# Optimization experiments

Measured on AMD Instinct MI355X. Metric: run time of the kernel, lower is better.

## Reference

```python
import math
import jax, jax.numpy as jnp
import numpy as np

B, C, H, W = 8, 256, 32, 32
NH, DK, DV = 8, 32, 32
EPS = 1e-6


def mish(x):
    return x * jnp.tanh(jax.nn.softplus(x))


def grouped_conv1x1(x, w, b, groups):
    # x: (B, Cin, N); w: (Cout, Cin//groups); b: (Cout,)
    Bb, Cin, N = x.shape
    Cout = w.shape[0]
    xg = x.reshape(Bb, groups, Cin // groups, N)
    wg = w.reshape(groups, Cout // groups, Cin // groups)
    y = jnp.einsum('bgin,goi->bgon', xg, wg).reshape(Bb, Cout, N)
    return y + b[None, :, None]


def conv_block(x, w, b, s, beta, groups):
    # 1x1 conv -> BatchNorm (eval: running mean 0 / var 1 => affine) -> Mish
    y = grouped_conv1x1(x, w, b, groups)
    y = s[None, :, None] * y + beta[None, :, None]
    return mish(y)


def setup_inputs() -> dict:
    key = jax.random.key(0)
    ks = jax.random.split(key, 8)
    inp = {
        'x': jax.random.normal(ks[0], (B, C, H, W), dtype=jnp.float32),
        'q_w': jax.random.normal(ks[1], (NH * DK, C // NH), dtype=jnp.float32) * 0.05,
        'q_b': jnp.zeros((NH * DK,), jnp.float32),
        'q_s': jnp.ones((NH * DK,), jnp.float32),
        'q_beta': jnp.zeros((NH * DK,), jnp.float32),
        'k_w': jax.random.normal(ks[2], (NH * DK, C // NH), dtype=jnp.float32) * 0.05,
        'k_b': jnp.zeros((NH * DK,), jnp.float32),
        'k_s': jnp.ones((NH * DK,), jnp.float32),
        'k_beta': jnp.zeros((NH * DK,), jnp.float32),
        'v_w': jax.random.normal(ks[3], (NH * DV, C // NH), dtype=jnp.float32) * 0.05,
        'v_b': jnp.zeros((NH * DV,), jnp.float32),
        'v_s': jnp.ones((NH * DV,), jnp.float32),
        'v_beta': jnp.zeros((NH * DV,), jnp.float32),
        'f_w': jax.random.normal(ks[4], (C, NH * DV), dtype=jnp.float32) * 0.05,
        'f_b': jnp.zeros((C,), jnp.float32),
        'f_s': jnp.ones((C,), jnp.float32),
        'f_beta': jnp.zeros((C,), jnp.float32),
    }
    return inp


def _forward(x, q_w, q_b, q_s, q_beta, k_w, k_b, k_s, k_beta,
             v_w, v_b, v_s, v_beta, f_w, f_b, f_s, f_beta):
    b, c, h, w = x.shape
    n = h * w
    temp = math.sqrt(c / NH)
    xf = x.reshape(b, c, n)

    q = conv_block(xf, q_w, q_b, q_s, q_beta, NH).reshape(b, NH, DK, n) / temp
    k = conv_block(xf, k_w, k_b, k_s, k_beta, NH).reshape(b, NH, DK, n)
    v = conv_block(xf, v_w, v_b, v_s, v_beta, NH).reshape(b, NH, DV, n)

    # cosine-distance attention (all heads vectorized); identical math to the
    # torch broadcast/repeat version but computed via normalized dot products.
    qn = jnp.sqrt(jnp.sum(q * q, axis=2))  # (b, nh, n)
    kn = jnp.sqrt(jnp.sum(k * k, axis=2))
    dot = jnp.einsum('bhdn,bhdm->bhnm', q, k)  # (b, nh, n, n)
    denom = jnp.maximum(qn[:, :, :, None] * kn[:, :, None, :], EPS)
    cos = jnp.clip(dot / denom, -1.0 + 1e-6, 1.0 - 1e-6)
    attn = jax.nn.softmax(1.0 - jnp.arccos(cos) / math.pi, axis=-1)

    # out[..., d, i] = sum_m v[..., d, m] * attn[..., i, m]
    out = jnp.einsum('bhdm,bhnm->bhdn', v, attn).reshape(b, NH * DV, n)

    y = conv_block(out, f_w, f_b, f_s, f_beta, 1).reshape(b, c, h, w) + x

    # extract_attn_map (no_grad in original)
    am = jnp.sum(jnp.mean(attn, axis=1), axis=1)  # (b, n)
    mn = jnp.min(am, axis=1, keepdims=True)
    mx = jnp.max(am, axis=1, keepdims=True)
    am = ((am - mn) / (mx - mn)).reshape(b, h, w)
    return y, jax.lax.stop_gradient(am)


def reference(x, q_w, q_b, q_s, q_beta, k_w, k_b, k_s, k_beta,
              v_w, v_b, v_s, v_beta, f_w, f_b, f_s, f_beta):
    return _forward(x, q_w, q_b, q_s, q_beta, k_w, k_b, k_s, k_beta,
                    v_w, v_b, v_s, v_beta, f_w, f_b, f_s, f_beta)
```

## Files before the change

kernel.cpp:

```cpp
#include <hip/hip_runtime.h>
#include <math.h>

#define B_   8
#define C_   256
#define NH_  8
#define N_   1024
#define LOG2E    1.4426950408889634f

typedef __attribute__((ext_vector_type(8))) short bf16x8;
typedef __attribute__((ext_vector_type(4))) float f32x4;
typedef __attribute__((ext_vector_type(2))) float f32x2;
typedef unsigned short u16;
typedef unsigned int u32;

#define AS1 __attribute__((address_space(1)))
#define AS3 __attribute__((address_space(3)))

__device__ __forceinline__ f32x4 mfma16(bf16x8 a, bf16x8 b, f32x4 c) {
    return __builtin_amdgcn_mfma_f32_16x16x32_bf16(a, b, c, 0, 0, 0);
}
__device__ __forceinline__ u32 bf16r(float x) {
    u32 b = __float_as_uint(x);
    return (b + 0x7fffu + ((b >> 16) & 1u)) >> 16;
}
__device__ __forceinline__ float mish_fast(float x) {
    float e  = __builtin_amdgcn_exp2f(fminf(x, 30.f) * LOG2E);
    float nm = e * (e + 2.f);
    return x * nm * __builtin_amdgcn_rcpf(nm + 2.f);
}
__device__ __forceinline__ f32x2 splat2(float v) { return (f32x2){v, v}; }
__device__ __forceinline__ f32x2 fexp_poly2(f32x2 c) {
    c = __builtin_elementwise_min(
            __builtin_elementwise_max(c, splat2(-0.999999f)), splat2(0.999999f));
    f32x2 u = c * c;
    f32x2 p = __builtin_elementwise_fma(splat2(1.7809920f), u, splat2(-3.7571968f));
    f32x2 q = __builtin_elementwise_fma(splat2(6.3713280f), u, splat2(-15.1427584f));
    p = __builtin_elementwise_fma(p, u, splat2(2.8140000f));
    q = __builtin_elementwise_fma(q, u, splat2(13.1518784f));
    p = __builtin_elementwise_fma(p, u, splat2(-0.8122592f));
    q = __builtin_elementwise_fma(q, u, splat2(-4.8903712f));
    p = __builtin_elementwise_fma(p, u, splat2(0.1705120f));
    q = __builtin_elementwise_fma(q, u, splat2(0.8441120f));
    p = __builtin_elementwise_fma(p, u, splat2(1.6473155f));
    q = __builtin_elementwise_fma(q, u, splat2(0.4936541f));
    return __builtin_elementwise_fma(c, q, p);
}

__global__ __launch_bounds__(256) void qkvpack_kernel(
    const float* __restrict__ x,
    const float* __restrict__ qw, const float* __restrict__ qb2,
    const float* __restrict__ qs, const float* __restrict__ qbeta,
    const float* __restrict__ kw, const float* __restrict__ kb2,
    const float* __restrict__ ks, const float* __restrict__ kbeta,
    const float* __restrict__ vw, const float* __restrict__ vb2,
    const float* __restrict__ vs, const float* __restrict__ vbeta,
    uint4* __restrict__ qpk, uint4* __restrict__ kpk, u16* __restrict__ vbf,
    const float* __restrict__ fw, u16* __restrict__ wbf)
{
    int blk = blockIdx.x;
    if (blk >= 768) {
        int id = (blk - 768) * 1024 + threadIdx.x;
#pragma unroll
        for (int j = 0; j < 4; ++j) { int p = id + j * 256; wbf[p] = (u16)bf16r(fw[p]); }
        return;
    }
    int type = blk >> 8;
    int sub = blk & 255;
    int nt = sub & 3, g = (sub >> 2) & 7, b = sub >> 5;
    int n = nt * 256 + threadIdx.x;
    int bh = b * 8 + g;
    const float* xp = x + ((size_t)b * C_ + g * 32) * N_ + n;
    float xv[32];
#pragma unroll
    for (int i = 0; i < 32; ++i) xv[i] = xp[(size_t)i * N_];

    const float *w, *bb, *sc, *bt;
    if (type == 0)      { w = qw; bb = qb2; sc = qs; bt = qbeta; }
    else if (type == 1) { w = kw; bb = kb2; sc = ks; bt = kbeta; }
    else                { w = vw; bb = vb2; sc = vs; bt = vbeta; }

    float y[32];
#pragma unroll
    for (int co = 0; co < 32; ++co) {
        int cg = g * 32 + co;
        float acc = 0.f;
#pragma unroll
        for (int i = 0; i < 32; ++i)
            acc = fmaf(xv[i], w[cg * 32 + i], acc);
        y[co] = mish_fast(sc[cg] * (acc + bb[cg]) + bt[cg]);
    }

    if (type == 2) {
#pragma unroll
        for (int co = 0; co < 32; ++co)
            vbf[((size_t)bh * 32 + co) * N_ + n] = (u16)bf16r(y[co]);
        return;
    }
    float s2 = 0.f;
#pragma unroll
    for (int d = 0; d < 32; ++d) s2 = fmaf(y[d], y[d], s2);
    float inv = __builtin_amdgcn_rsqf(fmaxf(s2, 1e-24f));
    u32 wp[16];
#pragma unroll
    for (int d = 0; d < 16; ++d)
        wp[d] = bf16r(y[2 * d] * inv) | (bf16r(y[2 * d + 1] * inv) << 16);
    uint4* dst = (type == 0 ? qpk : kpk) + ((size_t)bh * N_ + n) * 4;
#pragma unroll
    for (int j = 0; j < 4; ++j)
        dst[j] = make_uint4(wp[4 * j], wp[4 * j + 1], wp[4 * j + 2], wp[4 * j + 3]);
}

__global__ __launch_bounds__(256) void attn_kernel(
    const u16* __restrict__ qpk, const u16* __restrict__ kpk,
    const u16* __restrict__ vbf,
    u16* __restrict__ aout_bt, float* __restrict__ ampart)
{
    __shared__ __align__(16) u16 Kc[512 * 8];
    __shared__ __align__(16) u16 Vc[512 * 8];
    __shared__ __align__(16) u16 Ps[4][16 * 136];

    const int tid  = threadIdx.x;
    const int wave = tid >> 6, lane = tid & 63;
    const int l15 = lane & 15, lg = lane >> 4;
    const int swz = (blockIdx.x & 7) * 128 + (blockIdx.x >> 3);
    const int itile = swz & 15, bh = swz >> 4;
    const int h = bh & 7, bidx = bh >> 3;
    const int i0 = itile * 64;

    const char* ksrc = (const char*)(kpk + (size_t)bh * N_ * 32);
    const char* vsrc = (const char*)(vbf + (size_t)bh * 32 * N_);
    const char* qsrc = (const char*)(qpk + (size_t)bh * N_ * 32);

    const int kj0 = tid >> 7, km0g = tid & 127;
    const int kj1 = (256 + tid) >> 7, km1g = (256 + tid) & 127;
    const int vd0 = tid >> 4, vg0 = tid & 15;
    const int vd1 = (256 + tid) >> 4, vg1 = (256 + tid) & 15;
    const size_t koff0 = (size_t)km0g * 64 + kj0 * 16;
    const size_t koff1 = (size_t)km1g * 64 + kj1 * 16;
    const size_t voff0 = (size_t)vd0 * 2048 + ((vg0 ^ (vd0 & 7)) << 4);
    const size_t voff1 = (size_t)vd1 * 2048 + ((vg1 ^ (vd1 & 7)) << 4);

    bf16x8 aq = *(const bf16x8*)(qsrc + (size_t)(i0 + wave * 16 + l15) * 64 + lg * 16);

    const char* kfb = (const char*)Kc + lg * 2048 + l15 * 16;

    uint4 kreg0 = *(const uint4*)(ksrc + koff0);
    uint4 kreg1 = *(const uint4*)(ksrc + koff1);
    f32x2 rsL = {0.f, 0.f}, rsH = {0.f, 0.f};
    for (int ch = 0; ch < 8; ++ch) {
        *(uint4*)((char*)Kc + tid * 16)         = kreg0;
        *(uint4*)((char*)Kc + (256 + tid) * 16) = kreg1;
        if (ch < 7) {
            kreg0 = *(const uint4*)(ksrc + (size_t)(ch + 1) * 8192 + koff0);
            kreg1 = *(const uint4*)(ksrc + (size_t)(ch + 1) * 8192 + koff1);
        }
        asm volatile("s_waitcnt lgkmcnt(0)" ::: "memory");
        __builtin_amdgcn_sched_barrier(0);
        __builtin_amdgcn_s_barrier();
        __builtin_amdgcn_sched_barrier(0);
#pragma unroll
        for (int t = 0; t < 8; ++t) {
            bf16x8 bk = *(const bf16x8*)(kfb + t * 256);
            f32x4 cf = {0.f, 0.f, 0.f, 0.f};
            cf = mfma16(aq, bk, cf);
            rsL += fexp_poly2((f32x2){cf[0], cf[1]});
            rsH += fexp_poly2((f32x2){cf[2], cf[3]});
        }
        asm volatile("s_waitcnt lgkmcnt(0)" ::: "memory");
        __builtin_amdgcn_sched_barrier(0);
        __builtin_amdgcn_s_barrier();
        __builtin_amdgcn_sched_barrier(0);
    }
    float rinv[4];
    {
        float rr[4] = {rsL.x, rsL.y, rsH.x, rsH.y};
#pragma unroll
        for (int r = 0; r < 4; ++r) {
            float s = rr[r];
            s += __shfl_xor(s, 1); s += __shfl_xor(s, 2);
            s += __shfl_xor(s, 4); s += __shfl_xor(s, 8);
            rinv[r] = __builtin_amdgcn_rcpf(s);
        }
    }
    f32x2 rinvL = {rinv[0], rinv[1]}, rinvH = {rinv[2], rinv[3]};

    f32x4 o0 = {0.f, 0.f, 0.f, 0.f}, o1 = {0.f, 0.f, 0.f, 0.f};
    char*       psw = (char*)&Ps[wave][0] + lg * 1088 + l15 * 2;
    const char* pab = (const char*)&Ps[wave][0] + l15 * 272 + lg * 16;
    const char* vfb = (const char*)Vc + l15 * 256;
    const int   vkey = l15 & 7;
    float* amrow = ampart + (size_t)(swz * 4 + wave) * N_;

    kreg0 = *(const uint4*)(ksrc + koff0);
    kreg1 = *(const uint4*)(ksrc + koff1);
    uint4 vreg0 = *(const uint4*)(vsrc + voff0);
    uint4 vreg1 = *(const uint4*)(vsrc + voff1);

    for (int ch = 0; ch < 8; ++ch) {
        int m0 = ch * 128;
        *(uint4*)((char*)Kc + tid * 16)         = kreg0;
        *(uint4*)((char*)Kc + (256 + tid) * 16) = kreg1;
        *(uint4*)((char*)Vc + tid * 16)         = vreg0;
        *(uint4*)((char*)Vc + (256 + tid) * 16) = vreg1;
        if (ch < 7) {
            kreg0 = *(const uint4*)(ksrc + (size_t)(ch + 1) * 8192 + koff0);
            kreg1 = *(const uint4*)(ksrc + (size_t)(ch + 1) * 8192 + koff1);
            vreg0 = *(const uint4*)(vsrc + (size_t)(ch + 1) * 256 + voff0);
            vreg1 = *(const uint4*)(vsrc + (size_t)(ch + 1) * 256 + voff1);
        }
        asm volatile("s_waitcnt lgkmcnt(0)" ::: "memory");
        __builtin_amdgcn_sched_barrier(0);
        __builtin_amdgcn_s_barrier();
        __builtin_amdgcn_sched_barrier(0);

#pragma unroll
        for (int t = 0; t < 8; ++t) {
            bf16x8 bk = *(const bf16x8*)(kfb + t * 256);
            f32x4 cf = {0.f, 0.f, 0.f, 0.f};
            cf = mfma16(aq, bk, cf);
            f32x2 fL = fexp_poly2((f32x2){cf[0], cf[1]});
            f32x2 fH = fexp_poly2((f32x2){cf[2], cf[3]});
            *(u16*)(psw + 0 * 272 + t * 32) = (u16)bf16r(fL.x);
            *(u16*)(psw + 1 * 272 + t * 32) = (u16)bf16r(fL.y);
            *(u16*)(psw + 2 * 272 + t * 32) = (u16)bf16r(fH.x);
            *(u16*)(psw + 3 * 272 + t * 32) = (u16)bf16r(fH.y);
            f32x2 cs2 = fL * rinvL;
            cs2 = __builtin_elementwise_fma(fH, rinvH, cs2);
            float csum = cs2.x + cs2.y;
            csum += __shfl_xor(csum, 16);
            csum += __shfl_xor(csum, 32);
            if (lane < 16) amrow[m0 + t * 16 + l15] = csum;
        }
        asm volatile("s_waitcnt lgkmcnt(0)" ::: "memory");
        __builtin_amdgcn_sched_barrier(0);
#pragma unroll
        for (int kss = 0; kss < 4; ++kss) {
            bf16x8 pa = *(const bf16x8*)(pab + kss * 64);
            const char* va = vfb + (((kss * 4 + lg) ^ vkey) << 4);
            bf16x8 v0 = *(const bf16x8*)va;
            bf16x8 v1 = *(const bf16x8*)(va + 4096);
            o0 = mfma16(pa, v0, o0);
            o1 = mfma16(pa, v1, o1);
        }
        asm volatile("s_waitcnt lgkmcnt(0)" ::: "memory");
        __builtin_amdgcn_sched_barrier(0);
        __builtin_amdgcn_s_barrier();
        __builtin_amdgcn_sched_barrier(0);
    }

    {
        u16* oT = (u16*)Ps;
#pragma unroll
        for (int r = 0; r < 4; ++r) {
            int irow = wave * 16 + lg * 4 + r;
            oT[irow * 40 + l15]      = (u16)bf16r(o0[r] * rinv[r]);
            oT[irow * 40 + 16 + l15] = (u16)bf16r(o1[r] * rinv[r]);
        }
    }
    __syncthreads();
    {
        const u16* oT = (const u16*)Ps;
        int row = tid >> 2, c4 = tid & 3;
        uint4 val = *(const uint4*)((const char*)oT + row * 80 + c4 * 16);
        int n = i0 + row;
        int g = h * 4 + c4;
        size_t dst = ((size_t)(bidx * N_ + n) << 9) + ((size_t)((g ^ (row & 7)) << 4));
        *(uint4*)((char*)aout_bt + dst) = val;
    }
}

__global__ __launch_bounds__(256) void fconv_kernel(
    const u16* __restrict__ aout_bt, const u16* __restrict__ wbf,
    const float* __restrict__ x,
    const float* __restrict__ fs, const float* __restrict__ fb,
    const float* __restrict__ fbeta, float* __restrict__ y,
    const float* __restrict__ ampart, float* __restrict__ outAm)
{
    __shared__ __align__(16) u16 As[32 * 256];
    __shared__ float rmn[256], rmx[256];
    const int tid = threadIdx.x;

    if (blockIdx.x >= 256) {
        int b = blockIdx.x - 256;
        const float* base = ampart + (size_t)b * 512 * N_;
        float s[4] = {0.f, 0.f, 0.f, 0.f};
        for (int p = 0; p < 512; ++p) {
#pragma unroll
            for (int c2 = 0; c2 < 4; ++c2)
                s[c2] += base[(size_t)p * N_ + tid + 256 * c2];
        }
        float mn = fminf(fminf(s[0], s[1]), fminf(s[2], s[3]));
        float mx = fmaxf(fmaxf(s[0], s[1]), fmaxf(s[2], s[3]));
        rmn[tid] = mn; rmx[tid] = mx;
        __syncthreads();
        for (int off = 128; off >= 1; off >>= 1) {
            if (tid < off) {
                rmn[tid] = fminf(rmn[tid], rmn[tid + off]);
                rmx[tid] = fmaxf(rmx[tid], rmx[tid + off]);
            }
            __syncthreads();
        }
        mn = rmn[0]; mx = rmx[0];
        float inv = 1.f / (mx - mn);
#pragma unroll
        for (int c2 = 0; c2 < 4; ++c2)
            outAm[(size_t)b * N_ + tid + 256 * c2] = (s[c2] - mn) * inv;
        return;
    }

    const int wave = tid >> 6, lane = tid & 63;
    const int l15 = lane & 15, lg = lane >> 4;
    const int b  = blockIdx.x >> 5;
    const int n0 = (blockIdx.x & 31) * 32;

    const char* asrc = (const char*)aout_bt + ((size_t)(b * N_ + n0) << 9);
#pragma unroll
    for (int p = 0; p < 4; ++p) {
        int g = p * 256 + wave * 64 + lane;
        __builtin_amdgcn_global_load_lds(
            (const AS1 void*)(asrc + g * 16),
            (AS3 void*)((char*)As + ((p * 256 + wave * 64) << 4)), 16, 0, 0);
    }
    __syncthreads();

    f32x4 acc[4][2];
#pragma unroll
    for (int f = 0; f < 4; ++f)
#pragma unroll
        for (int fn = 0; fn < 2; ++fn) acc[f][fn] = (f32x4){0.f, 0.f, 0.f, 0.f};

    const int cobase = wave * 64;
#pragma unroll
    for (int kk = 0; kk < 8; ++kk) {
        bf16x8 af[2];
#pragma unroll
        for (int fn = 0; fn < 2; ++fn) {
            int nf = fn * 16 + l15;
            af[fn] = *(const bf16x8*)((const char*)As + nf * 512 +
                                      (((kk * 4 + lg) ^ (nf & 7)) << 4));
        }
#pragma unroll
        for (int f = 0; f < 4; ++f) {
            bf16x8 wf = *(const bf16x8*)(wbf + (size_t)(cobase + f * 16 + l15) * 256 + kk * 32 + lg * 8);
            acc[f][0] = mfma16(wf, af[0], acc[f][0]);
            acc[f][1] = mfma16(wf, af[1], acc[f][1]);
        }
    }

#pragma unroll
    for (int f = 0; f < 4; ++f) {
#pragma unroll
        for (int r = 0; r < 4; ++r) {
            int co = cobase + f * 16 + lg * 4 + r;
            float sc = fs[co], bb = fb[co], bt = fbeta[co];
#pragma unroll
            for (int fn = 0; fn < 2; ++fn) {
                int n = n0 + fn * 16 + l15;
                size_t oid = ((size_t)(b * C_ + co) << 10) + n;
                y[oid] = mish_fast(sc * (acc[f][fn][r] + bb) + bt) + x[oid];
            }
        }
    }
}

extern "C" void kernel_launch(void* const* d_in, const int* in_sizes, int n_in,
                              void* d_out, int out_size, void* d_ws, size_t ws_size,
                              hipStream_t stream)
{
    const float* x     = (const float*)d_in[0];
    const float* q_w   = (const float*)d_in[1];
    const float* q_b   = (const float*)d_in[2];
    const float* q_s   = (const float*)d_in[3];
    const float* q_be  = (const float*)d_in[4];
    const float* k_w   = (const float*)d_in[5];
    const float* k_b   = (const float*)d_in[6];
    const float* k_s   = (const float*)d_in[7];
    const float* k_be  = (const float*)d_in[8];
    const float* v_w   = (const float*)d_in[9];
    const float* v_b   = (const float*)d_in[10];
    const float* v_s   = (const float*)d_in[11];
    const float* v_be  = (const float*)d_in[12];
    const float* f_w   = (const float*)d_in[13];
    const float* f_b   = (const float*)d_in[14];
    const float* f_s   = (const float*)d_in[15];
    const float* f_be  = (const float*)d_in[16];

    float* y_out  = (float*)d_out;
    float* am_out = (float*)d_out + (size_t)B_ * C_ * N_;

    char* w = (char*)d_ws;
    u16*   qpk     = (u16*)w;    w += (size_t)B_ * NH_ * N_ * 64;
    u16*   kpk     = (u16*)w;    w += (size_t)B_ * NH_ * N_ * 64;
    u16*   vbf     = (u16*)w;    w += (size_t)B_ * C_ * N_ * 2;
    u16*   aout_bt = (u16*)w;    w += (size_t)B_ * N_ * C_ * 2;
    float* ampart  = (float*)w;  w += (size_t)B_ * NH_ * 16 * 4 * N_ * 4;
    u16*   wbf     = (u16*)w;

    qkvpack_kernel<<<832, 256, 0, stream>>>(
        x, q_w, q_b, q_s, q_be, k_w, k_b, k_s, k_be,
        v_w, v_b, v_s, v_be, (uint4*)qpk, (uint4*)kpk, vbf, f_w, wbf);

    attn_kernel<<<B_ * NH_ * 16, 256, 0, stream>>>(
        qpk, kpk, vbf, aout_bt, ampart);

    fconv_kernel<<<264, 256, 0, stream>>>(
        aout_bt, wbf, x, f_s, f_b, f_be, y_out, ampart, am_out);
}
```

Baseline: 121.6 us.

## Cache exp scores in registers, share K/V LDS buffer, reduce attn map in LDS

The first pass over K now keeps the bf16-packed exponentiated scores in a 128-entry register array, so the second pass no longer reloads K or recomputes QK^T and the exponentials. It only streams V through a single shared LDS buffer that replaces the separate K and V buffers. Per-wave attention-map column sums are accumulated with LDS atomics into one row per block instead of four global rows. This cuts ampart writes and the fconv reduction loop by a factor of four. The main risk is the large register array raising VGPR pressure, possibly spilling or lowering occupancy, and the column sums now use bf16-rounded values.

```diff
diff --git a/kernel.cpp b/kernel.cpp
--- a/kernel.cpp
+++ b/kernel.cpp
@@ -115,9 +115,9 @@
     const u16* __restrict__ vbf,
     u16* __restrict__ aout_bt, float* __restrict__ ampart)
 {
-    __shared__ __align__(16) u16 Kc[512 * 8];
-    __shared__ __align__(16) u16 Vc[512 * 8];
+    __shared__ __align__(16) u16 KV[512 * 8];
     __shared__ __align__(16) u16 Ps[4][16 * 136];
+    __shared__ __align__(16) float amW[N_];
 
     const int tid  = threadIdx.x;
     const int wave = tid >> 6, lane = tid & 63;
@@ -130,6 +130,8 @@
     const char* ksrc = (const char*)(kpk + (size_t)bh * N_ * 32);
     const char* vsrc = (const char*)(vbf + (size_t)bh * 32 * N_);
     const char* qsrc = (const char*)(qpk + (size_t)bh * N_ * 32);
+
+    for (int j = tid; j < N_; j += 256) amW[j] = 0.f;
 
     const int kj0 = tid >> 7, km0g = tid & 127;
     const int kj1 = (256 + tid) >> 7, km1g = (256 + tid) & 127;
@@ -142,14 +144,17 @@
 
     bf16x8 aq = *(const bf16x8*)(qsrc + (size_t)(i0 + wave * 16 + l15) * 64 + lg * 16);
 
-    const char* kfb = (const char*)Kc + lg * 2048 + l15 * 16;
+    const char* kfb = (const char*)KV + lg * 2048 + l15 * 16;
+
+    u32 fc[128];
 
     uint4 kreg0 = *(const uint4*)(ksrc + koff0);
     uint4 kreg1 = *(const uint4*)(ksrc + koff1);
     f32x2 rsL = {0.f, 0.f}, rsH = {0.f, 0.f};
+#pragma unroll
     for (int ch = 0; ch < 8; ++ch) {
-        *(uint4*)((char*)Kc + tid * 16)         = kreg0;
-        *(uint4*)((char*)Kc + (256 + tid) * 16) = kreg1;
+        *(uint4*)((char*)KV + tid * 16)         = kreg0;
+        *(uint4*)((char*)KV + (256 + tid) * 16) = kreg1;
         if (ch < 7) {
             kreg0 = *(const uint4*)(ksrc + (size_t)(ch + 1) * 8192 + koff0);
             kreg1 = *(const uint4*)(ksrc + (size_t)(ch + 1) * 8192 + koff1);
@@ -158,61 +163,6 @@
         __builtin_amdgcn_sched_barrier(0);
         __builtin_amdgcn_s_barrier();
         __builtin_amdgcn_sched_barrier(0);
-#pragma unroll
-        for (int t = 0; t < 8; ++t) {
-            bf16x8 bk = *(const bf16x8*)(kfb + t * 256);
-            f32x4 cf = {0.f, 0.f, 0.f, 0.f};
-            cf = mfma16(aq, bk, cf);
-            rsL += fexp_poly2((f32x2){cf[0], cf[1]});
-            rsH += fexp_poly2((f32x2){cf[2], cf[3]});
-        }
-        asm volatile("s_waitcnt lgkmcnt(0)" ::: "memory");
-        __builtin_amdgcn_sched_barrier(0);
-        __builtin_amdgcn_s_barrier();
-        __builtin_amdgcn_sched_barrier(0);
-    }
-    float rinv[4];
-    {
-        float rr[4] = {rsL.x, rsL.y, rsH.x, rsH.y};
-#pragma unroll
-        for (int r = 0; r < 4; ++r) {
-            float s = rr[r];
-            s += __shfl_xor(s, 1); s += __shfl_xor(s, 2);
-            s += __shfl_xor(s, 4); s += __shfl_xor(s, 8);
-            rinv[r] = __builtin_amdgcn_rcpf(s);
-        }
-    }
-    f32x2 rinvL = {rinv[0], rinv[1]}, rinvH = {rinv[2], rinv[3]};
-
-    f32x4 o0 = {0.f, 0.f, 0.f, 0.f}, o1 = {0.f, 0.f, 0.f, 0.f};
-    char*       psw = (char*)&Ps[wave][0] + lg * 1088 + l15 * 2;
-    const char* pab = (const char*)&Ps[wave][0] + l15 * 272 + lg * 16;
-    const char* vfb = (const char*)Vc + l15 * 256;
-    const int   vkey = l15 & 7;
-    float* amrow = ampart + (size_t)(swz * 4 + wave) * N_;
-
-    kreg0 = *(const uint4*)(ksrc + koff0);
-    kreg1 = *(const uint4*)(ksrc + koff1);
-    uint4 vreg0 = *(const uint4*)(vsrc + voff0);
-    uint4 vreg1 = *(const uint4*)(vsrc + voff1);
-
-    for (int ch = 0; ch < 8; ++ch) {
-        int m0 = ch * 128;
-        *(uint4*)((char*)Kc + tid * 16)         = kreg0;
-        *(uint4*)((char*)Kc + (256 + tid) * 16) = kreg1;
-        *(uint4*)((char*)Vc + tid * 16)         = vreg0;
-        *(uint4*)((char*)Vc + (256 + tid) * 16) = vreg1;
-        if (ch < 7) {
-            kreg0 = *(const uint4*)(ksrc + (size_t)(ch + 1) * 8192 + koff0);
-            kreg1 = *(const uint4*)(ksrc + (size_t)(ch + 1) * 8192 + koff1);
-            vreg0 = *(const uint4*)(vsrc + (size_t)(ch + 1) * 256 + voff0);
-            vreg1 = *(const uint4*)(vsrc + (size_t)(ch + 1) * 256 + voff1);
-        }
-        asm volatile("s_waitcnt lgkmcnt(0)" ::: "memory");
-        __builtin_amdgcn_sched_barrier(0);
-        __builtin_amdgcn_s_barrier();
-        __builtin_amdgcn_sched_barrier(0);
-
 #pragma unroll
         for (int t = 0; t < 8; ++t) {
             bf16x8 bk = *(const bf16x8*)(kfb + t * 256);
@@ -220,16 +170,66 @@
             cf = mfma16(aq, bk, cf);
             f32x2 fL = fexp_poly2((f32x2){cf[0], cf[1]});
             f32x2 fH = fexp_poly2((f32x2){cf[2], cf[3]});
-            *(u16*)(psw + 0 * 272 + t * 32) = (u16)bf16r(fL.x);
-            *(u16*)(psw + 1 * 272 + t * 32) = (u16)bf16r(fL.y);
-            *(u16*)(psw + 2 * 272 + t * 32) = (u16)bf16r(fH.x);
-            *(u16*)(psw + 3 * 272 + t * 32) = (u16)bf16r(fH.y);
+            rsL += fL; rsH += fH;
+            fc[ch * 16 + t * 2]     = bf16r(fL.x) | (bf16r(fL.y) << 16);
+            fc[ch * 16 + t * 2 + 1] = bf16r(fH.x) | (bf16r(fH.y) << 16);
+        }
+        asm volatile("s_waitcnt lgkmcnt(0)" ::: "memory");
+        __builtin_amdgcn_sched_barrier(0);
+        __builtin_amdgcn_s_barrier();
+        __builtin_amdgcn_sched_barrier(0);
+    }
+    float rinv[4];
+    {
+        float rr[4] = {rsL.x, rsL.y, rsH.x, rsH.y};
+#pragma unroll
+        for (int r = 0; r < 4; ++r) {
+            float s = rr[r];
+            s += __shfl_xor(s, 1); s += __shfl_xor(s, 2);
+            s += __shfl_xor(s, 4); s += __shfl_xor(s, 8);
+            rinv[r] = __builtin_amdgcn_rcpf(s);
+        }
+    }
+    f32x2 rinvL = {rinv[0], rinv[1]}, rinvH = {rinv[2], rinv[3]};
+
+    f32x4 o0 = {0.f, 0.f, 0.f, 0.f}, o1 = {0.f, 0.f, 0.f, 0.f};
+    char*       psw = (char*)&Ps[wave][0] + lg * 1088 + l15 * 2;
+    const char* pab = (const char*)&Ps[wave][0] + l15 * 272 + lg * 16;
+    const char* vfb = (const char*)KV + l15 * 256;
+    const int   vkey = l15 & 7;
+
+    uint4 vreg0 = *(const uint4*)(vsrc + voff0);
+    uint4 vreg1 = *(const uint4*)(vsrc + voff1);
+
+#pragma unroll
+    for (int ch = 0; ch < 8; ++ch) {
+        *(uint4*)((char*)KV + tid * 16)         = vreg0;
+        *(uint4*)((char*)KV + (256 + tid) * 16) = vreg1;
+        if (ch < 7) {
+            vreg0 = *(const uint4*)(vsrc + (size_t)(ch + 1) * 256 + voff0);
+            vreg1 = *(const uint4*)(vsrc + (size_t)(ch + 1) * 256 + voff1);
+        }
+        asm volatile("s_waitcnt lgkmcnt(0)" ::: "memory");
+        __builtin_amdgcn_sched_barrier(0);
+        __builtin_amdgcn_s_barrier();
+        __builtin_amdgcn_sched_barrier(0);
+
+#pragma unroll
+        for (int t = 0; t < 8; ++t) {
+            u32 r0 = fc[ch * 16 + t * 2];
+            u32 r1 = fc[ch * 16 + t * 2 + 1];
+            *(u16*)(psw + 0 * 272 + t * 32) = (u16)r0;
+            *(u16*)(psw + 1 * 272 + t * 32) = (u16)(r0 >> 16);
+            *(u16*)(psw + 2 * 272 + t * 32) = (u16)r1;
+            *(u16*)(psw + 3 * 272 + t * 32) = (u16)(r1 >> 16);
+            f32x2 fL = {__uint_as_float(r0 << 16), __uint_as_float(r0 & 0xffff0000u)};
+            f32x2 fH = {__uint_as_float(r1 << 16), __uint_as_float(r1 & 0xffff0000u)};
             f32x2 cs2 = fL * rinvL;
             cs2 = __builtin_elementwise_fma(fH, rinvH, cs2);
             float csum = cs2.x + cs2.y;
             csum += __shfl_xor(csum, 16);
             csum += __shfl_xor(csum, 32);
-            if (lane < 16) amrow[m0 + t * 16 + l15] = csum;
+            if (lane < 16) atomicAdd(&amW[ch * 128 + t * 16 + l15], csum);
         }
         asm volatile("s_waitcnt lgkmcnt(0)" ::: "memory");
         __builtin_amdgcn_sched_barrier(0);
@@ -247,6 +247,7 @@
         __builtin_amdgcn_s_barrier();
         __builtin_amdgcn_sched_barrier(0);
     }
+    __syncthreads();
 
     {
         u16* oT = (u16*)Ps;
@@ -267,6 +268,9 @@
         size_t dst = ((size_t)(bidx * N_ + n) << 9) + ((size_t)((g ^ (row & 7)) << 4));
         *(uint4*)((char*)aout_bt + dst) = val;
     }
+#pragma unroll
+    for (int j2 = 0; j2 < 4; ++j2)
+        ampart[(size_t)swz * N_ + tid + 256 * j2] = amW[tid + 256 * j2];
 }
 
 __global__ __launch_bounds__(256) void fconv_kernel(
@@ -282,9 +286,9 @@
 
     if (blockIdx.x >= 256) {
         int b = blockIdx.x - 256;
-        const float* base = ampart + (size_t)b * 512 * N_;
+        const float* base = ampart + (size_t)b * 128 * N_;
         float s[4] = {0.f, 0.f, 0.f, 0.f};
-        for (int p = 0; p < 512; ++p) {
+        for (int p = 0; p < 128; ++p) {
 #pragma unroll
             for (int c2 = 0; c2 < 4; ++c2)
                 s[c2] += base[(size_t)p * N_ + tid + 256 * c2];
@@ -393,7 +397,7 @@
     u16*   kpk     = (u16*)w;    w += (size_t)B_ * NH_ * N_ * 64;
     u16*   vbf     = (u16*)w;    w += (size_t)B_ * C_ * N_ * 2;
     u16*   aout_bt = (u16*)w;    w += (size_t)B_ * N_ * C_ * 2;
-    float* ampart  = (float*)w;  w += (size_t)B_ * NH_ * 16 * 4 * N_ * 4;
+    float* ampart  = (float*)w;  w += (size_t)B_ * NH_ * 16 * N_ * 4;
     u16*   wbf     = (u16*)w;
 
     qkvpack_kernel<<<832, 256, 0, stream>>>(
```

Result: slower. 128.9 us (+6.0%).
